# Kernel tuning notes

Hardware: AMD Instinct MI355X
Metric: run time of the kernel (lower is better)

The kernel has to match this reference:

```python
import jax, jax.numpy as jnp
import numpy as np

PAD = 10000.0  # sentinel value marking invalid fg points


def setup_inputs() -> dict:
    key = jax.random.key(0)
    k1, k2, k3 = jax.random.split(key, 3)
    B, N, M, D = 8, 4096, 4096, 3
    fg = jax.random.normal(k1, (B, N, D), dtype=jnp.float32)
    prj = jax.random.normal(k2, (B, M, D), dtype=jnp.float32)
    # per-sample valid lengths in [1, N]; pad the tail rows with the sentinel
    x_lengths = jax.random.randint(k3, (B,), 1, N + 1)
    row_idx = jnp.arange(N)[None, :]              # [1, N]
    pad_mask = row_idx >= x_lengths[:, None]      # [B, N] True where padded
    fg = jnp.where(pad_mask[:, :, None], PAD, fg)
    return {"fg_points": fg, "prj_points": prj, "x_lengths": x_lengths}


def _chamfer(fg, prj):
    # fg: [B, N, 3] (padded with PAD rows), prj: [B, M, 3]
    valid = jnp.all(fg != PAD, axis=-1)  # [B, N]
    # squared pairwise distances via ||a||^2 + ||b||^2 - 2 a.b  -> [B, N, M]
    d2 = (jnp.sum(fg * fg, axis=-1)[:, :, None]
          + jnp.sum(prj * prj, axis=-1)[:, None, :]
          - 2.0 * jnp.einsum('bnd,bmd->bnm', fg, prj))
    d2 = jnp.maximum(d2, 0.0)
    n_valid = jnp.sum(valid, axis=1).astype(jnp.float32)  # [B]
    # x -> y: min over prj for each valid fg point, mean over valid points
    cham_x = jnp.sum(jnp.where(valid, jnp.min(d2, axis=2), 0.0), axis=1) / n_valid
    # y -> x: min over valid fg points for each prj point, mean over prj
    BIG = jnp.float32(1e30)
    cham_y = jnp.mean(jnp.min(jnp.where(valid[:, :, None], d2, BIG), axis=1), axis=1)
    # pytorch3d chamfer_distance (default reductions) = cham_x + cham_y per sample
    return jnp.mean(cham_x + cham_y)


def reference(fg_points, prj_points, x_lengths):
    fg = fg_points.astype(jnp.float32)
    prj = prj_points.astype(jnp.float32)
    _ = x_lengths.astype(jnp.int64)  # cast, unused (matches original)
    return _chamfer(fg, prj)
```

## Files before the change

### kernel.cpp

```cpp
#include <hip/hip_runtime.h>

#define TPB 256
#define PPT 8
#define WAVE_OWN (64 * PPT)
#define OWN_TILE (TPB * PPT)
#define CHUNK 128


__global__ __launch_bounds__(TPB) void cham_dist_kernel(
    const float* __restrict__ fg, const float* __restrict__ prj,
    const int* __restrict__ lengths,
    unsigned int* __restrict__ rowmin, unsigned int* __restrict__ colmin,
    int B, int N, int M,
    int tilesX, int chunksX, int tilesY, int chunksY)
{
    const int blocksX = B * tilesX * chunksX;
    int idx = blockIdx.x;
    const int side = (idx >= blocksX) ? 1 : 0;
    if (side) idx -= blocksX;
    const int tilesPer  = side ? tilesY  : tilesX;
    const int chunksPer = side ? chunksY : chunksX;
    const int b     = idx / (tilesPer * chunksPer);
    const int rem   = idx % (tilesPer * chunksPer);
    const int tile  = rem / chunksPer;
    const int chunk = rem % chunksPer;

    const float* own     = side ? prj : fg;
    const float* other   = side ? fg  : prj;
    unsigned int* outArr = side ? colmin : rowmin;
    const int ownCount   = side ? M : N;
    const int otherCount = side ? N : M;
    const int L          = lengths[b];

    const int start = chunk * CHUNK;
    int cnt = min(CHUNK, otherCount - start);
    if (side == 1) {
        if (start >= L) return;
        cnt = min(cnt, L - start);
    }

    __shared__ float4 tilebuf[CHUNK];
    if (threadIdx.x < cnt) {
        const float* q = other + ((size_t)b * otherCount + start + threadIdx.x) * 3;
        float bx = q[0], by = q[1], bz = q[2];
        tilebuf[threadIdx.x] = make_float4(bx, by, bz, bx * bx + by * by + bz * bz);
    }
    __syncthreads();

    const int lane  = threadIdx.x & 63;
    const int wave  = threadIdx.x >> 6;
    const int wbase = tile * OWN_TILE + wave * WAVE_OWN;
    if (wbase >= ownCount) return;
    if (side == 0 && wbase >= L) return;

    float m2x[PPT], m2y[PPT], m2z[PPT], aa[PPT], mn[PPT];
    #pragma unroll
    for (int p = 0; p < PPT; ++p) {
        int i  = wbase + p * 64 + lane;
        int li = min(i, ownCount - 1);
        const float* a = own + ((size_t)b * ownCount + li) * 3;
        float ax = a[0], ay = a[1], az = a[2];
        m2x[p] = -2.f * ax; m2y[p] = -2.f * ay; m2z[p] = -2.f * az;
        aa[p]  = ax * ax + ay * ay + az * az;
        mn[p]  = __int_as_float(0x7F800000);
    }

    int j = 0;
    #pragma unroll 2
    for (; j + 1 < cnt; j += 2) {
        float4 q0 = tilebuf[j];
        float4 q1 = tilebuf[j + 1];
        #pragma unroll
        for (int p = 0; p < PPT; ++p) {
            float t0 = fmaf(m2x[p], q0.x, q0.w);
            t0 = fmaf(m2y[p], q0.y, t0);
            t0 = fmaf(m2z[p], q0.z, t0);
            float t1 = fmaf(m2x[p], q1.x, q1.w);
            t1 = fmaf(m2y[p], q1.y, t1);
            t1 = fmaf(m2z[p], q1.z, t1);
            mn[p] = fminf(fminf(t0, t1), mn[p]);
        }
    }
    if (j < cnt) {
        float4 q0 = tilebuf[j];
        #pragma unroll
        for (int p = 0; p < PPT; ++p) {
            float t0 = fmaf(m2x[p], q0.x, q0.w);
            t0 = fmaf(m2y[p], q0.y, t0);
            t0 = fmaf(m2z[p], q0.z, t0);
            mn[p] = fminf(mn[p], t0);
        }
    }

    #pragma unroll
    for (int p = 0; p < PPT; ++p) {
        int i = wbase + p * 64 + lane;
        if (i < ownCount) {
            float v = fmaxf(mn[p] + aa[p], 0.f);
            atomicMin(&outArr[(size_t)b * ownCount + i], __float_as_uint(v));
        }
    }
}

__global__ __launch_bounds__(1024) void cham_reduce_kernel(
    const unsigned int* __restrict__ rowmin, const unsigned int* __restrict__ colmin,
    const int* __restrict__ lengths, float* __restrict__ out, int B, int N, int M)
{
    __shared__ float wavesum[16];
    const int b    = blockIdx.x;
    const int tid  = threadIdx.x;
    const int lane = tid & 63;
    const int wave = tid >> 6;

    const int L = lengths[b];
    float sx = 0.f, sy = 0.f;
    for (int n = tid; n < L; n += 1024) sx += __uint_as_float(rowmin[(size_t)b * N + n]);
    for (int m = tid; m < M; m += 1024) sy += __uint_as_float(colmin[(size_t)b * M + m]);
    float v = sx / (float)L + sy / (float)M;
    #pragma unroll
    for (int off = 32; off > 0; off >>= 1) v += __shfl_down(v, off, 64);
    if (lane == 0) wavesum[wave] = v;
    __syncthreads();
    if (tid == 0) {
        float t = 0.f;
        #pragma unroll
        for (int w = 0; w < 16; ++w) t += wavesum[w];
        atomicAdd(out, t / (float)B);
    }
}

extern "C" void kernel_launch(void* const* d_in, const int* in_sizes, int n_in,
                              void* d_out, int out_size, void* d_ws, size_t ws_size,
                              hipStream_t stream) {
    const float* fg      = (const float*)d_in[0];
    const float* prj     = (const float*)d_in[1];
    const int*   lengths = (const int*)d_in[2];
    float*       out     = (float*)d_out;

    const int B = in_sizes[2];
    const int N = in_sizes[0] / (3 * B);
    const int M = in_sizes[1] / (3 * B);

    unsigned int* rowmin = (unsigned int*)d_ws;
    unsigned int* colmin = rowmin + (size_t)B * N;

    const int tilesX  = (N + OWN_TILE - 1) / OWN_TILE;
    const int chunksX = (M + CHUNK - 1) / CHUNK;
    const int tilesY  = (M + OWN_TILE - 1) / OWN_TILE;
    const int chunksY = (N + CHUNK - 1) / CHUNK;
    const int totalBlocks = B * (tilesX * chunksX + tilesY * chunksY);
    cham_dist_kernel<<<totalBlocks, TPB, 0, stream>>>(
        fg, prj, lengths, rowmin, colmin, B, N, M, tilesX, chunksX, tilesY, chunksY);

    cham_reduce_kernel<<<B, 1024, 0, stream>>>(rowmin, colmin, lengths, out, B, N, M);
}
```

Baseline: 77.46 us.

## Use single-wave blocks for chamfer distance and split reduction across sub-blocks

The distance kernel now runs one 64-thread wave per block instead of four waves sharing a staged chunk. Each block skips early when its whole tile is padding, which removes the idle waves that 256-thread blocks carried on fully padded tiles. The inner loop unrolls four points per step and the tail loop handles any remainder. The reduction spreads each batch over 8 blocks of 256 threads to get more parallelism, at the cost of more atomic adds to the output and four times as many dist blocks, each staging its chunk itself.

```diff
diff --git a/kernel.cpp b/kernel.cpp
--- a/kernel.cpp
+++ b/kernel.cpp
@@ -1,13 +1,12 @@
 #include <hip/hip_runtime.h>
 
-#define TPB 256
+#define TPB 64
 #define PPT 8
-#define WAVE_OWN (64 * PPT)
-#define OWN_TILE (TPB * PPT)
+#define WAVE_OWN (TPB * PPT)
 #define CHUNK 128
 
 
-__global__ __launch_bounds__(TPB) void cham_dist_kernel(
+__global__ __launch_bounds__(TPB, 4) void cham_dist_kernel(
     const float* __restrict__ fg, const float* __restrict__ prj,
     const int* __restrict__ lengths,
     unsigned int* __restrict__ rowmin, unsigned int* __restrict__ colmin,
@@ -32,6 +31,10 @@
     const int otherCount = side ? N : M;
     const int L          = lengths[b];
 
+    const int wbase = tile * WAVE_OWN;
+    if (wbase >= ownCount) return;
+    if (side == 0 && wbase >= L) return;
+
     const int start = chunk * CHUNK;
     int cnt = min(CHUNK, otherCount - start);
     if (side == 1) {
@@ -39,20 +42,16 @@
         cnt = min(cnt, L - start);
     }
 
+    const int lane = threadIdx.x;
+
     __shared__ float4 tilebuf[CHUNK];
-    if (threadIdx.x < cnt) {
-        const float* q = other + ((size_t)b * otherCount + start + threadIdx.x) * 3;
+    for (int t = lane; t < cnt; t += TPB) {
+        const float* q = other + ((size_t)b * otherCount + start + t) * 3;
         float bx = q[0], by = q[1], bz = q[2];
-        tilebuf[threadIdx.x] = make_float4(bx, by, bz, bx * bx + by * by + bz * bz);
+        tilebuf[t] = make_float4(bx, by, bz, bx * bx + by * by + bz * bz);
     }
-    __syncthreads();
 
-    const int lane  = threadIdx.x & 63;
-    const int wave  = threadIdx.x >> 6;
-    const int wbase = tile * OWN_TILE + wave * WAVE_OWN;
-    if (wbase >= ownCount) return;
-    if (side == 0 && wbase >= L) return;
-
+    const int lim = side ? ownCount : min(ownCount, L);
     float m2x[PPT], m2y[PPT], m2z[PPT], aa[PPT], mn[PPT];
     #pragma unroll
     for (int p = 0; p < PPT; ++p) {
@@ -64,12 +63,14 @@
         aa[p]  = ax * ax + ay * ay + az * az;
         mn[p]  = __int_as_float(0x7F800000);
     }
+    __syncthreads();
 
     int j = 0;
-    #pragma unroll 2
-    for (; j + 1 < cnt; j += 2) {
+    for (; j + 3 < cnt; j += 4) {
         float4 q0 = tilebuf[j];
         float4 q1 = tilebuf[j + 1];
+        float4 q2 = tilebuf[j + 2];
+        float4 q3 = tilebuf[j + 3];
         #pragma unroll
         for (int p = 0; p < PPT; ++p) {
             float t0 = fmaf(m2x[p], q0.x, q0.w);
@@ -79,9 +80,16 @@
             t1 = fmaf(m2y[p], q1.y, t1);
             t1 = fmaf(m2z[p], q1.z, t1);
             mn[p] = fminf(fminf(t0, t1), mn[p]);
+            float t2 = fmaf(m2x[p], q2.x, q2.w);
+            t2 = fmaf(m2y[p], q2.y, t2);
+            t2 = fmaf(m2z[p], q2.z, t2);
+            float t3 = fmaf(m2x[p], q3.x, q3.w);
+            t3 = fmaf(m2y[p], q3.y, t3);
+            t3 = fmaf(m2z[p], q3.z, t3);
+            mn[p] = fminf(fminf(t2, t3), mn[p]);
         }
     }
-    if (j < cnt) {
+    for (; j < cnt; ++j) {
         float4 q0 = tilebuf[j];
         #pragma unroll
         for (int p = 0; p < PPT; ++p) {
@@ -95,37 +103,42 @@
     #pragma unroll
     for (int p = 0; p < PPT; ++p) {
         int i = wbase + p * 64 + lane;
-        if (i < ownCount) {
+        if (i < lim) {
             float v = fmaxf(mn[p] + aa[p], 0.f);
             atomicMin(&outArr[(size_t)b * ownCount + i], __float_as_uint(v));
         }
     }
 }
 
-__global__ __launch_bounds__(1024) void cham_reduce_kernel(
+#define RSUB 8
+#define RTPB 256
+__global__ __launch_bounds__(RTPB) void cham_reduce_kernel(
     const unsigned int* __restrict__ rowmin, const unsigned int* __restrict__ colmin,
     const int* __restrict__ lengths, float* __restrict__ out, int B, int N, int M)
 {
-    __shared__ float wavesum[16];
-    const int b    = blockIdx.x;
+    __shared__ float wavesum[RTPB / 64];
+    const int b    = blockIdx.x / RSUB;
+    const int sub  = blockIdx.x % RSUB;
     const int tid  = threadIdx.x;
     const int lane = tid & 63;
     const int wave = tid >> 6;
+    const int t      = sub * RTPB + tid;
+    const int STRIDE = RSUB * RTPB;
 
     const int L = lengths[b];
     float sx = 0.f, sy = 0.f;
-    for (int n = tid; n < L; n += 1024) sx += __uint_as_float(rowmin[(size_t)b * N + n]);
-    for (int m = tid; m < M; m += 1024) sy += __uint_as_float(colmin[(size_t)b * M + m]);
+    for (int n = t; n < L; n += STRIDE) sx += __uint_as_float(rowmin[(size_t)b * N + n]);
+    for (int m = t; m < M; m += STRIDE) sy += __uint_as_float(colmin[(size_t)b * M + m]);
     float v = sx / (float)L + sy / (float)M;
     #pragma unroll
     for (int off = 32; off > 0; off >>= 1) v += __shfl_down(v, off, 64);
     if (lane == 0) wavesum[wave] = v;
     __syncthreads();
     if (tid == 0) {
-        float t = 0.f;
+        float tsum = 0.f;
         #pragma unroll
-        for (int w = 0; w < 16; ++w) t += wavesum[w];
-        atomicAdd(out, t / (float)B);
+        for (int w = 0; w < RTPB / 64; ++w) tsum += wavesum[w];
+        atomicAdd(out, tsum / (float)B);
     }
 }
 
@@ -144,13 +157,13 @@
     unsigned int* rowmin = (unsigned int*)d_ws;
     unsigned int* colmin = rowmin + (size_t)B * N;
 
-    const int tilesX  = (N + OWN_TILE - 1) / OWN_TILE;
+    const int tilesX  = (N + WAVE_OWN - 1) / WAVE_OWN;
     const int chunksX = (M + CHUNK - 1) / CHUNK;
-    const int tilesY  = (M + OWN_TILE - 1) / OWN_TILE;
+    const int tilesY  = (M + WAVE_OWN - 1) / WAVE_OWN;
     const int chunksY = (N + CHUNK - 1) / CHUNK;
     const int totalBlocks = B * (tilesX * chunksX + tilesY * chunksY);
     cham_dist_kernel<<<totalBlocks, TPB, 0, stream>>>(
         fg, prj, lengths, rowmin, colmin, B, N, M, tilesX, chunksX, tilesY, chunksY);
 
-    cham_reduce_kernel<<<B, 1024, 0, stream>>>(rowmin, colmin, lengths, out, B, N, M);
+    cham_reduce_kernel<<<B * RSUB, RTPB, 0, stream>>>(rowmin, colmin, lengths, out, B, N, M);
 }
```

After: 78.13 us. No clear change (+0.9%).
